# Kernel tuning notes

Measured on AMD Instinct MI355X. Metric: run time of the kernel, lower is better.

## Reference

```python
import jax, jax.numpy as jnp
import numpy as np
import math

D_MODEL = 1024
N_HEADS = 16
D_HEAD = D_MODEL // N_HEADS


def setup_inputs() -> dict:
    key = jax.random.key(0)
    ks = jax.random.split(key, 5)
    B, T, C = 4, 2048, D_MODEL
    s = 1.0 / math.sqrt(C)
    return {
        "x": jax.random.normal(ks[0], (B, T, C), dtype=jnp.float32),
        "qkv_w": jax.random.normal(ks[1], (3 * C, C), dtype=jnp.float32) * s,
        "qkv_b": jnp.zeros((3 * C,), dtype=jnp.float32),
        "out_w": jax.random.normal(ks[2], (C, C), dtype=jnp.float32) * s,
        "out_b": jnp.zeros((C,), dtype=jnp.float32),
    }


def reference(x, qkv_w, qkv_b, out_w, out_b):
    B, T, C = x.shape
    H, Dh = N_HEADS, D_HEAD
    qkv = x @ qkv_w.T + qkv_b              # [B,T,3C] (torch Linear: x W^T + b)
    q, k, v = jnp.split(qkv, 3, axis=-1)
    # [B,T,C] -> [B,H,T,Dh]
    q = q.reshape(B, T, H, Dh).transpose(0, 2, 1, 3)
    k = k.reshape(B, T, H, Dh).transpose(0, 2, 1, 3)
    v = v.reshape(B, T, H, Dh).transpose(0, 2, 1, 3)
    att = jnp.einsum("bhqd,bhkd->bhqk", q, k) / math.sqrt(Dh)
    causal = jnp.tril(jnp.ones((T, T), dtype=bool))  # True = keep
    att = jnp.where(causal, att, -jnp.inf)
    att = jax.nn.softmax(att, axis=-1)
    y = jnp.einsum("bhqk,bhkd->bhqd", att, v)
    y = y.transpose(0, 2, 1, 3).reshape(B, T, C)
    return y @ out_w.T + out_b
```

## Files before the change

### kernel.cpp

```cpp
#include <hip/hip_runtime.h>

typedef __attribute__((ext_vector_type(4))) float f32x4;
typedef __attribute__((ext_vector_type(16))) float f32x16;
typedef __attribute__((ext_vector_type(8))) __bf16 bf16x8;
typedef __attribute__((ext_vector_type(4))) __bf16 bf16x4;
typedef __attribute__((ext_vector_type(2))) unsigned u32x2;

#define MFMA_B16(a,b,c) __builtin_amdgcn_mfma_f32_16x16x32_bf16((a),(b),(c),0,0,0)
#define MFMA32(a,b,c)  __builtin_amdgcn_mfma_f32_32x32x16_bf16((a),(b),(c),0,0,0)

static constexpr int T_LEN  = 2048;
static constexpr int C_DIM  = 1024;
static constexpr int H_NUM  = 16;
static constexpr int D_HEADc = 64;
static constexpr float Q_PRESCALE = 0.125f * 1.4426950408889634f;

__device__ __forceinline__ void async16(const void* g, void* l) {
  __builtin_amdgcn_global_load_lds(
      (const __attribute__((address_space(1))) unsigned int*)g,
      (__attribute__((address_space(3))) unsigned int*)l, 16, 0, 0);
}

__device__ __forceinline__ unsigned cvtpk(float lo, float hi) {
  unsigned r;
  asm("v_cvt_pk_bf16_f32 %0, %1, %2" : "=v"(r) : "v"(lo), "v"(hi));
  return r;
}

__global__ __launch_bounds__(256) void cvt_kernel(const float* __restrict__ s,
                                                  __bf16* __restrict__ d, int n4) {
  int i = blockIdx.x * 256 + threadIdx.x;
  if (i >= n4) return;
  float4 f = reinterpret_cast<const float4*>(s)[i];
  bf16x4 o;
  o.x = (__bf16)f.x; o.y = (__bf16)f.y; o.z = (__bf16)f.z; o.w = (__bf16)f.w;
  reinterpret_cast<bf16x4*>(d)[i] = o;
}

__global__ __launch_bounds__(256) void gemm_qkv(const __bf16* __restrict__ A,
                                                const __bf16* __restrict__ W,
                                                const float* __restrict__ bias,
                                                __bf16* __restrict__ qb,
                                                __bf16* __restrict__ kb,
                                                __bf16* __restrict__ vb) {
  constexpr int K = 1024;
  __shared__ __bf16 As[128 * 64];
  __shared__ __bf16 Bs[128 * 64];
  const int tid = threadIdx.x;
  const int wid = tid >> 6, lane = tid & 63, l16 = lane & 15, lg = lane >> 4;
  const int r8 = lane >> 3, sl = lane & 7;
  const int r7 = l16 & 7;
  const int wm = wid >> 1, wn = wid & 1;
  const int m0 = blockIdx.x * 128, n0 = blockIdx.y * 128;

  f32x4 acc[4][4];
#pragma unroll
  for (int i = 0; i < 4; ++i)
#pragma unroll
    for (int j = 0; j < 4; ++j) acc[i][j] = f32x4{0.f, 0.f, 0.f, 0.f};

  for (int k0 = 0; k0 < K; k0 += 64) {
    __builtin_amdgcn_s_barrier();
#pragma unroll
    for (int it = 0; it < 4; ++it) {
      int chunk = it * 4 + wid;
      int row = chunk * 8 + r8;
      int scol = ((sl ^ (row & 7)) << 3);
      async16(A + (long)(m0 + row) * K + k0 + scol, &As[chunk * 512]);
      async16(W + (long)(n0 + row) * K + k0 + scol, &Bs[chunk * 512]);
    }
    asm volatile("s_waitcnt vmcnt(0)" ::: "memory");
    __builtin_amdgcn_s_barrier();
#pragma unroll
    for (int kt = 0; kt < 2; ++kt) {
      const int sw = ((((kt << 2) | lg) ^ r7) << 3);
      bf16x8 af[4], bfv[4];
#pragma unroll
      for (int mi = 0; mi < 4; ++mi)
        af[mi] = *reinterpret_cast<const bf16x8*>(&As[(wm * 64 + mi * 16 + l16) * 64 + sw]);
#pragma unroll
      for (int nt = 0; nt < 4; ++nt)
        bfv[nt] = *reinterpret_cast<const bf16x8*>(&Bs[(wn * 64 + nt * 16 + l16) * 64 + sw]);
#pragma unroll
      for (int mi = 0; mi < 4; ++mi)
#pragma unroll
        for (int nt = 0; nt < 4; ++nt)
          acc[mi][nt] = MFMA_B16(af[mi], bfv[nt], acc[mi][nt]);
    }
  }
#pragma unroll
  for (int mi = 0; mi < 4; ++mi)
#pragma unroll
    for (int nt = 0; nt < 4; ++nt)
#pragma unroll
      for (int r = 0; r < 4; ++r) {
        int m = m0 + wm * 64 + mi * 16 + lg * 4 + r;
        int n = n0 + wn * 64 + nt * 16 + l16;
        float val = acc[mi][nt][r] + bias[n];
        int which = n >> 10;
        int cc = n & 1023;
        int h = cc >> 6, d = cc & 63;
        long b = m >> 11;
        long t = m & 2047;
        if (which == 0) {
          qb[(((b * H_NUM + h) * T_LEN) + t) * D_HEADc + d] = (__bf16)(val * Q_PRESCALE);
        } else if (which == 1) {
          kb[(((b * H_NUM + h) * T_LEN) + t) * D_HEADc + d] = (__bf16)val;
        } else {
          vb[(((b * H_NUM + h) * D_HEADc) + d) * T_LEN + t] = (__bf16)val;
        }
      }
}

__global__ __launch_bounds__(256) void attn_kernel(const __bf16* __restrict__ q,
                                                   const __bf16* __restrict__ k,
                                                   const __bf16* __restrict__ vt,
                                                   __bf16* __restrict__ y) {
  __shared__ __bf16 Ks[2][64 * 64];
  __shared__ __bf16 Vs[2][64 * 64];
  const int tid = threadIdx.x;
  const int wid = tid >> 6, lane = tid & 63;
  const int l31 = lane & 31, hi = lane >> 5;
  const int r8 = lane >> 3, sl = lane & 7;
  const int r7 = l31 & 7;
  const int bid = blockIdx.x;
  const int qt = 15 - (bid >> 6);
  const int bh = bid & 63;
  const int q0 = qt * 128;
  const int qw = q0 + wid * 32;
  const int qglob = qw + l31;
  const __bf16* qg = q + (long)bh * T_LEN * D_HEADc;
  const __bf16* kg = k + (long)bh * T_LEN * D_HEADc;
  const __bf16* vg = vt + (long)bh * T_LEN * D_HEADc;

  bf16x8 qf[4];
#pragma unroll
  for (int dt = 0; dt < 4; ++dt)
    qf[dt] = *reinterpret_cast<const bf16x8*>(
        qg + (long)qglob * D_HEADc + dt * 16 + hi * 8);

  f32x16 o[2];
#pragma unroll
  for (int di = 0; di < 2; ++di)
#pragma unroll
    for (int r = 0; r < 16; ++r) o[di][r] = 0.f;
  float m = -3e38f, l = 0.f;

  auto stage = [&](int buf, int t) {
    const int k0s = t * 64;
#pragma unroll
    for (int it = 0; it < 2; ++it) {
      int chunk = it * 4 + wid;
      int row = chunk * 8 + r8;
      int scol = ((sl ^ (row & 7)) << 3);
      async16(kg + (long)(k0s + row) * D_HEADc + scol, &Ks[buf][chunk * 512]);
      async16(vg + (long)row * T_LEN + k0s + scol, &Vs[buf][chunk * 512]);
    }
  };

  const int ntiles = qt * 2 + 2;
  stage(0, 0);
  int cur = 0;
  for (int t = 0; t < ntiles; ++t) {
    if (t + 1 < ntiles) {
      stage(cur ^ 1, t + 1);
      asm volatile("s_waitcnt vmcnt(4)" ::: "memory");
    } else {
      asm volatile("s_waitcnt vmcnt(0)" ::: "memory");
    }
    __builtin_amdgcn_s_barrier();
    const int k0 = t * 64;
    if (k0 < qw + 32) {
      f32x16 s[2];
#pragma unroll
      for (int ki = 0; ki < 2; ++ki)
#pragma unroll
        for (int r = 0; r < 16; ++r) s[ki][r] = 0.f;
      __builtin_amdgcn_s_setprio(1);
#pragma unroll
      for (int dt = 0; dt < 4; ++dt) {
        const int swz = (((dt << 1) | hi) ^ r7) << 3;
        bf16x8 kf0 = *reinterpret_cast<const bf16x8*>(&Ks[cur][l31 * 64 + swz]);
        bf16x8 kf1 = *reinterpret_cast<const bf16x8*>(&Ks[cur][(32 + l31) * 64 + swz]);
        s[0] = MFMA32(kf0, qf[dt], s[0]);
        s[1] = MFMA32(kf1, qf[dt], s[1]);
      }
      __builtin_amdgcn_s_setprio(0);

      if (k0 + 63 > qw) {
#pragma unroll
        for (int r = 0; r < 16; ++r) {
          const int kb = (r & 3) + 8 * (r >> 2) + 4 * hi;
          if (k0 + kb > qglob) s[0][r] = -3e38f;
          if (k0 + 32 + kb > qglob) s[1][r] = -3e38f;
        }
      }
      float mx = -3e38f;
#pragma unroll
      for (int r = 0; r < 16; ++r) mx = fmaxf(mx, fmaxf(s[0][r], s[1][r]));
      mx = fmaxf(mx, __shfl_xor(mx, 32));
      if (!__all(mx <= m + 8.f)) {
        const float mn = fmaxf(m, mx);
        const float al = exp2f(m - mn);
        m = mn;
        l *= al;
#pragma unroll
        for (int di = 0; di < 2; ++di)
#pragma unroll
          for (int r = 0; r < 16; ++r) o[di][r] *= al;
      }
      float ls = 0.f;
      unsigned pb[4][4];
#pragma unroll
      for (int ki = 0; ki < 2; ++ki) {
#pragma unroll
        for (int r = 0; r < 16; ++r) {
          float e = exp2f(s[ki][r] - m);
          ls += e;
          s[ki][r] = e;
        }
        unsigned d0 = cvtpk(s[ki][0], s[ki][1]),   d1 = cvtpk(s[ki][2], s[ki][3]);
        unsigned d2 = cvtpk(s[ki][4], s[ki][5]),   d3 = cvtpk(s[ki][6], s[ki][7]);
        unsigned d4 = cvtpk(s[ki][8], s[ki][9]),   d5 = cvtpk(s[ki][10], s[ki][11]);
        unsigned d6 = cvtpk(s[ki][12], s[ki][13]), d7 = cvtpk(s[ki][14], s[ki][15]);
        u32x2 a = __builtin_amdgcn_permlane32_swap(d0, d2, false, false);
        u32x2 b = __builtin_amdgcn_permlane32_swap(d1, d3, false, false);
        pb[ki * 2][0] = a[0]; pb[ki * 2][1] = b[0];
        pb[ki * 2][2] = a[1]; pb[ki * 2][3] = b[1];
        u32x2 c = __builtin_amdgcn_permlane32_swap(d4, d6, false, false);
        u32x2 d = __builtin_amdgcn_permlane32_swap(d5, d7, false, false);
        pb[ki * 2 + 1][0] = c[0]; pb[ki * 2 + 1][1] = d[0];
        pb[ki * 2 + 1][2] = c[1]; pb[ki * 2 + 1][3] = d[1];
      }
      ls += __shfl_xor(ls, 32);
      l += ls;

      __builtin_amdgcn_s_setprio(1);
#pragma unroll
      for (int kt = 0; kt < 4; ++kt) {
        union { unsigned u[4]; bf16x8 v; } pu;
        pu.u[0] = pb[kt][0]; pu.u[1] = pb[kt][1];
        pu.u[2] = pb[kt][2]; pu.u[3] = pb[kt][3];
        const int swz = (((kt << 1) | hi) ^ r7) << 3;
        bf16x8 vf0 = *reinterpret_cast<const bf16x8*>(&Vs[cur][l31 * 64 + swz]);
        bf16x8 vf1 = *reinterpret_cast<const bf16x8*>(&Vs[cur][(32 + l31) * 64 + swz]);
        o[0] = MFMA32(vf0, pu.v, o[0]);
        o[1] = MFMA32(vf1, pu.v, o[1]);
      }
      __builtin_amdgcn_s_setprio(0);
    }
    __builtin_amdgcn_s_barrier();
    cur ^= 1;
  }

  const long bb = bh >> 4;
  const int h = bh & 15;
  const float inv = 1.f / l;
  const long row = bb * T_LEN + qglob;
#pragma unroll
  for (int di = 0; di < 2; ++di)
#pragma unroll
    for (int rr = 0; rr < 4; ++rr) {
      bf16x4 pk;
#pragma unroll
      for (int c = 0; c < 4; ++c) pk[c] = (__bf16)(o[di][rr * 4 + c] * inv);
      *reinterpret_cast<bf16x4*>(
          &y[row * C_DIM + h * D_HEADc + di * 32 + rr * 8 + hi * 4]) = pk;
    }
}

__global__ __launch_bounds__(256) void gemm_proj(const __bf16* __restrict__ A,
                                                 const __bf16* __restrict__ W,
                                                 const float* __restrict__ bias,
                                                 float* __restrict__ out) {
  constexpr int K = 1024;
  __shared__ __bf16 As[128 * 64];
  __shared__ __bf16 Bs[128 * 64];
  const int tid = threadIdx.x;
  const int wid = tid >> 6, lane = tid & 63, l16 = lane & 15, lg = lane >> 4;
  const int r8 = lane >> 3, sl = lane & 7;
  const int r7 = l16 & 7;
  const int wm = wid >> 1, wn = wid & 1;
  const int m0 = blockIdx.x * 128, n0 = blockIdx.y * 128;

  f32x4 acc[4][4];
#pragma unroll
  for (int i = 0; i < 4; ++i)
#pragma unroll
    for (int j = 0; j < 4; ++j) acc[i][j] = f32x4{0.f, 0.f, 0.f, 0.f};

  for (int k0 = 0; k0 < K; k0 += 64) {
    __builtin_amdgcn_s_barrier();
#pragma unroll
    for (int it = 0; it < 4; ++it) {
      int chunk = it * 4 + wid;
      int row = chunk * 8 + r8;
      int scol = ((sl ^ (row & 7)) << 3);
      async16(A + (long)(m0 + row) * K + k0 + scol, &As[chunk * 512]);
      async16(W + (long)(n0 + row) * K + k0 + scol, &Bs[chunk * 512]);
    }
    asm volatile("s_waitcnt vmcnt(0)" ::: "memory");
    __builtin_amdgcn_s_barrier();
#pragma unroll
    for (int kt = 0; kt < 2; ++kt) {
      const int sw = ((((kt << 2) | lg) ^ r7) << 3);
      bf16x8 af[4], bfv[4];
#pragma unroll
      for (int mi = 0; mi < 4; ++mi)
        af[mi] = *reinterpret_cast<const bf16x8*>(&As[(wm * 64 + mi * 16 + l16) * 64 + sw]);
#pragma unroll
      for (int nt = 0; nt < 4; ++nt)
        bfv[nt] = *reinterpret_cast<const bf16x8*>(&Bs[(wn * 64 + nt * 16 + l16) * 64 + sw]);
#pragma unroll
      for (int mi = 0; mi < 4; ++mi)
#pragma unroll
        for (int nt = 0; nt < 4; ++nt)
          acc[mi][nt] = MFMA_B16(af[mi], bfv[nt], acc[mi][nt]);
    }
  }
#pragma unroll
  for (int mi = 0; mi < 4; ++mi)
#pragma unroll
    for (int nt = 0; nt < 4; ++nt)
#pragma unroll
      for (int r = 0; r < 4; ++r) {
        long m = m0 + wm * 64 + mi * 16 + lg * 4 + r;
        int n = n0 + wn * 64 + nt * 16 + l16;
        out[m * C_DIM + n] = acc[mi][nt][r] + bias[n];
      }
}

extern "C" void kernel_launch(void* const* d_in, const int* in_sizes, int n_in,
                              void* d_out, int out_size, void* d_ws, size_t ws_size,
                              hipStream_t stream) {
  const float* x     = (const float*)d_in[0];
  const float* qkv_w = (const float*)d_in[1];
  const float* qkv_b = (const float*)d_in[2];
  const float* out_w = (const float*)d_in[3];
  const float* out_b = (const float*)d_in[4];
  float* out = (float*)d_out;

  const long NX  = 8192L * 1024;
  const long NWQ = 3072L * 1024;
  const long NWO = 1024L * 1024;
  const size_t need = (size_t)(5 * NX + NWQ + NWO) * 2;
  if (ws_size < need) return;

  __bf16* xb   = (__bf16*)d_ws;
  __bf16* wqkv = xb + NX;
  __bf16* wout = wqkv + NWQ;
  __bf16* qb   = wout + NWO;
  __bf16* kb   = qb + NX;
  __bf16* vb   = kb + NX;
  __bf16* yb   = vb + NX;

  cvt_kernel<<<(int)(NX / 4 / 256), 256, 0, stream>>>(x, xb, (int)(NX / 4));
  cvt_kernel<<<(int)(NWQ / 4 / 256), 256, 0, stream>>>(qkv_w, wqkv, (int)(NWQ / 4));
  cvt_kernel<<<(int)(NWO / 4 / 256), 256, 0, stream>>>(out_w, wout, (int)(NWO / 4));

  gemm_qkv<<<dim3(64, 24), 256, 0, stream>>>(xb, wqkv, qkv_b, qb, kb, vb);
  attn_kernel<<<dim3(1024), 256, 0, stream>>>(qb, kb, vb, yb);
  gemm_proj<<<dim3(64, 8), 256, 0, stream>>>(yb, wout, out_b, out);
}
```

Before: 196.4 us.

## Double attention query tile per block, fuse conversion kernels, tree-reduce softmax

Each attention warp now processes 64 query rows as two 32-row sub-blocks that share the K and V fragments loaded from LDS. The query tile per block grows to 256, which halves the grid and halves K/V staging traffic per query. The three fp32-to-bf16 conversion launches are merged into one kernel, and the softmax max and sum reductions become tree reductions. In exchange, register pressure roughly doubles, occupancy may fall, and the block count drops to 512, which may leave the causal workload less evenly balanced across CUs.

```diff
diff --git a/kernel.cpp b/kernel.cpp
--- a/kernel.cpp
+++ b/kernel.cpp
@@ -27,14 +27,21 @@
   return r;
 }
 
-__global__ __launch_bounds__(256) void cvt_kernel(const float* __restrict__ s,
-                                                  __bf16* __restrict__ d, int n4) {
+__global__ __launch_bounds__(256) void cvt3_kernel(const float* __restrict__ a, __bf16* __restrict__ da, int na,
+                                                   const float* __restrict__ b, __bf16* __restrict__ db, int nb,
+                                                   const float* __restrict__ c, __bf16* __restrict__ dc, int nc) {
   int i = blockIdx.x * 256 + threadIdx.x;
-  if (i >= n4) return;
-  float4 f = reinterpret_cast<const float4*>(s)[i];
+  const float* s;
+  __bf16* d;
+  long j;
+  if (i < na) { s = a; d = da; j = i; }
+  else if (i < na + nb) { s = b; d = db; j = i - na; }
+  else if (i < na + nb + nc) { s = c; d = dc; j = i - na - nb; }
+  else return;
+  float4 f = reinterpret_cast<const float4*>(s)[j];
   bf16x4 o;
   o.x = (__bf16)f.x; o.y = (__bf16)f.y; o.z = (__bf16)f.z; o.w = (__bf16)f.w;
-  reinterpret_cast<bf16x4*>(d)[i] = o;
+  reinterpret_cast<bf16x4*>(d)[j] = o;
 }
 
 __global__ __launch_bounds__(256) void gemm_qkv(const __bf16* __restrict__ A,
@@ -124,27 +131,29 @@
   const int r8 = lane >> 3, sl = lane & 7;
   const int r7 = l31 & 7;
   const int bid = blockIdx.x;
-  const int qt = 15 - (bid >> 6);
+  const int qt = 7 - (bid >> 6);
   const int bh = bid & 63;
-  const int q0 = qt * 128;
-  const int qw = q0 + wid * 32;
-  const int qglob = qw + l31;
+  const int q0 = qt * 256;
+  const int qw = q0 + wid * 64;
+  const int qgA = qw + l31;
+  const int qgB = qw + 32 + l31;
   const __bf16* qg = q + (long)bh * T_LEN * D_HEADc;
   const __bf16* kg = k + (long)bh * T_LEN * D_HEADc;
   const __bf16* vg = vt + (long)bh * T_LEN * D_HEADc;
 
-  bf16x8 qf[4];
-#pragma unroll
-  for (int dt = 0; dt < 4; ++dt)
-    qf[dt] = *reinterpret_cast<const bf16x8*>(
-        qg + (long)qglob * D_HEADc + dt * 16 + hi * 8);
-
-  f32x16 o[2];
+  bf16x8 qfA[4], qfB[4];
+#pragma unroll
+  for (int dt = 0; dt < 4; ++dt) {
+    qfA[dt] = *reinterpret_cast<const bf16x8*>(qg + (long)qgA * D_HEADc + dt * 16 + hi * 8);
+    qfB[dt] = *reinterpret_cast<const bf16x8*>(qg + (long)qgB * D_HEADc + dt * 16 + hi * 8);
+  }
+
+  f32x16 oA[2], oB[2];
 #pragma unroll
   for (int di = 0; di < 2; ++di)
 #pragma unroll
-    for (int r = 0; r < 16; ++r) o[di][r] = 0.f;
-  float m = -3e38f, l = 0.f;
+    for (int r = 0; r < 16; ++r) { oA[di][r] = 0.f; oB[di][r] = 0.f; }
+  float mA = -3e38f, lA = 0.f, mB = -3e38f, lB = 0.f;
 
   auto stage = [&](int buf, int t) {
     const int k0s = t * 64;
@@ -158,7 +167,66 @@
     }
   };
 
-  const int ntiles = qt * 2 + 2;
+  auto softmax_block = [&](f32x16* s, float& m, float& l, f32x16* o,
+                           unsigned (&pb)[4][4], int qgl, int qwl, int k0) {
+    if (k0 + 63 > qwl) {
+#pragma unroll
+      for (int r = 0; r < 16; ++r) {
+        const int kb = (r & 3) + 8 * (r >> 2) + 4 * hi;
+        if (k0 + kb > qgl) s[0][r] = -3e38f;
+        if (k0 + 32 + kb > qgl) s[1][r] = -3e38f;
+      }
+    }
+    float v8[8];
+#pragma unroll
+    for (int r = 0; r < 8; ++r)
+      v8[r] = fmaxf(fmaxf(s[0][r], s[0][r + 8]), fmaxf(s[1][r], s[1][r + 8]));
+#pragma unroll
+    for (int st = 4; st > 0; st >>= 1)
+#pragma unroll
+      for (int r = 0; r < st; ++r) v8[r] = fmaxf(v8[r], v8[r + st]);
+    float mx = fmaxf(v8[0], __shfl_xor(v8[0], 32));
+    if (!__all(mx <= m + 8.f)) {
+      const float mn = fmaxf(m, mx);
+      const float al = exp2f(m - mn);
+      m = mn;
+      l *= al;
+#pragma unroll
+      for (int di = 0; di < 2; ++di)
+#pragma unroll
+        for (int r = 0; r < 16; ++r) o[di][r] *= al;
+    }
+#pragma unroll
+    for (int ki = 0; ki < 2; ++ki)
+#pragma unroll
+      for (int r = 0; r < 16; ++r) s[ki][r] = exp2f(s[ki][r] - m);
+    float t8[8];
+#pragma unroll
+    for (int r = 0; r < 8; ++r)
+      t8[r] = (s[0][r] + s[0][r + 8]) + (s[1][r] + s[1][r + 8]);
+#pragma unroll
+    for (int st = 4; st > 0; st >>= 1)
+#pragma unroll
+      for (int r = 0; r < st; ++r) t8[r] += t8[r + st];
+    l += t8[0] + __shfl_xor(t8[0], 32);
+#pragma unroll
+    for (int ki = 0; ki < 2; ++ki) {
+      unsigned d0 = cvtpk(s[ki][0], s[ki][1]),   d1 = cvtpk(s[ki][2], s[ki][3]);
+      unsigned d2 = cvtpk(s[ki][4], s[ki][5]),   d3 = cvtpk(s[ki][6], s[ki][7]);
+      unsigned d4 = cvtpk(s[ki][8], s[ki][9]),   d5 = cvtpk(s[ki][10], s[ki][11]);
+      unsigned d6 = cvtpk(s[ki][12], s[ki][13]), d7 = cvtpk(s[ki][14], s[ki][15]);
+      u32x2 a2 = __builtin_amdgcn_permlane32_swap(d0, d2, false, false);
+      u32x2 b2 = __builtin_amdgcn_permlane32_swap(d1, d3, false, false);
+      pb[ki * 2][0] = a2[0]; pb[ki * 2][1] = b2[0];
+      pb[ki * 2][2] = a2[1]; pb[ki * 2][3] = b2[1];
+      u32x2 c2 = __builtin_amdgcn_permlane32_swap(d4, d6, false, false);
+      u32x2 e2 = __builtin_amdgcn_permlane32_swap(d5, d7, false, false);
+      pb[ki * 2 + 1][0] = c2[0]; pb[ki * 2 + 1][1] = e2[0];
+      pb[ki * 2 + 1][2] = c2[1]; pb[ki * 2 + 1][3] = e2[1];
+    }
+  };
+
+  const int ntiles = (qt + 1) * 4;
   stage(0, 0);
   int cur = 0;
   for (int t = 0; t < ntiles; ++t) {
@@ -170,82 +238,42 @@
     }
     __builtin_amdgcn_s_barrier();
     const int k0 = t * 64;
-    if (k0 < qw + 32) {
-      f32x16 s[2];
+    if (k0 < qw + 64) {
+      f32x16 sA[2], sB[2];
 #pragma unroll
       for (int ki = 0; ki < 2; ++ki)
 #pragma unroll
-        for (int r = 0; r < 16; ++r) s[ki][r] = 0.f;
+        for (int r = 0; r < 16; ++r) { sA[ki][r] = 0.f; sB[ki][r] = 0.f; }
       __builtin_amdgcn_s_setprio(1);
 #pragma unroll
       for (int dt = 0; dt < 4; ++dt) {
         const int swz = (((dt << 1) | hi) ^ r7) << 3;
         bf16x8 kf0 = *reinterpret_cast<const bf16x8*>(&Ks[cur][l31 * 64 + swz]);
         bf16x8 kf1 = *reinterpret_cast<const bf16x8*>(&Ks[cur][(32 + l31) * 64 + swz]);
-        s[0] = MFMA32(kf0, qf[dt], s[0]);
-        s[1] = MFMA32(kf1, qf[dt], s[1]);
+        sA[0] = MFMA32(kf0, qfA[dt], sA[0]);
+        sA[1] = MFMA32(kf1, qfA[dt], sA[1]);
+        sB[0] = MFMA32(kf0, qfB[dt], sB[0]);
+        sB[1] = MFMA32(kf1, qfB[dt], sB[1]);
       }
       __builtin_amdgcn_s_setprio(0);
 
-      if (k0 + 63 > qw) {
-#pragma unroll
-        for (int r = 0; r < 16; ++r) {
-          const int kb = (r & 3) + 8 * (r >> 2) + 4 * hi;
-          if (k0 + kb > qglob) s[0][r] = -3e38f;
-          if (k0 + 32 + kb > qglob) s[1][r] = -3e38f;
-        }
-      }
-      float mx = -3e38f;
-#pragma unroll
-      for (int r = 0; r < 16; ++r) mx = fmaxf(mx, fmaxf(s[0][r], s[1][r]));
-      mx = fmaxf(mx, __shfl_xor(mx, 32));
-      if (!__all(mx <= m + 8.f)) {
-        const float mn = fmaxf(m, mx);
-        const float al = exp2f(m - mn);
-        m = mn;
-        l *= al;
-#pragma unroll
-        for (int di = 0; di < 2; ++di)
-#pragma unroll
-          for (int r = 0; r < 16; ++r) o[di][r] *= al;
-      }
-      float ls = 0.f;
-      unsigned pb[4][4];
-#pragma unroll
-      for (int ki = 0; ki < 2; ++ki) {
-#pragma unroll
-        for (int r = 0; r < 16; ++r) {
-          float e = exp2f(s[ki][r] - m);
-          ls += e;
-          s[ki][r] = e;
-        }
-        unsigned d0 = cvtpk(s[ki][0], s[ki][1]),   d1 = cvtpk(s[ki][2], s[ki][3]);
-        unsigned d2 = cvtpk(s[ki][4], s[ki][5]),   d3 = cvtpk(s[ki][6], s[ki][7]);
-        unsigned d4 = cvtpk(s[ki][8], s[ki][9]),   d5 = cvtpk(s[ki][10], s[ki][11]);
-        unsigned d6 = cvtpk(s[ki][12], s[ki][13]), d7 = cvtpk(s[ki][14], s[ki][15]);
-        u32x2 a = __builtin_amdgcn_permlane32_swap(d0, d2, false, false);
-        u32x2 b = __builtin_amdgcn_permlane32_swap(d1, d3, false, false);
-        pb[ki * 2][0] = a[0]; pb[ki * 2][1] = b[0];
-        pb[ki * 2][2] = a[1]; pb[ki * 2][3] = b[1];
-        u32x2 c = __builtin_amdgcn_permlane32_swap(d4, d6, false, false);
-        u32x2 d = __builtin_amdgcn_permlane32_swap(d5, d7, false, false);
-        pb[ki * 2 + 1][0] = c[0]; pb[ki * 2 + 1][1] = d[0];
-        pb[ki * 2 + 1][2] = c[1]; pb[ki * 2 + 1][3] = d[1];
-      }
-      ls += __shfl_xor(ls, 32);
-      l += ls;
+      unsigned pbA[4][4], pbB[4][4];
+      softmax_block(sA, mA, lA, oA, pbA, qgA, qw, k0);
+      softmax_block(sB, mB, lB, oB, pbB, qgB, qw + 32, k0);
 
       __builtin_amdgcn_s_setprio(1);
 #pragma unroll
       for (int kt = 0; kt < 4; ++kt) {
-        union { unsigned u[4]; bf16x8 v; } pu;
-        pu.u[0] = pb[kt][0]; pu.u[1] = pb[kt][1];
-        pu.u[2] = pb[kt][2]; pu.u[3] = pb[kt][3];
+        union { unsigned u[4]; bf16x8 v; } puA, puB;
+#pragma unroll
+        for (int w = 0; w < 4; ++w) { puA.u[w] = pbA[kt][w]; puB.u[w] = pbB[kt][w]; }
         const int swz = (((kt << 1) | hi) ^ r7) << 3;
         bf16x8 vf0 = *reinterpret_cast<const bf16x8*>(&Vs[cur][l31 * 64 + swz]);
         bf16x8 vf1 = *reinterpret_cast<const bf16x8*>(&Vs[cur][(32 + l31) * 64 + swz]);
-        o[0] = MFMA32(vf0, pu.v, o[0]);
-        o[1] = MFMA32(vf1, pu.v, o[1]);
+        oA[0] = MFMA32(vf0, puA.v, oA[0]);
+        oA[1] = MFMA32(vf1, puA.v, oA[1]);
+        oB[0] = MFMA32(vf0, puB.v, oB[0]);
+        oB[1] = MFMA32(vf1, puB.v, oB[1]);
       }
       __builtin_amdgcn_s_setprio(0);
     }
@@ -255,17 +283,20 @@
 
   const long bb = bh >> 4;
   const int h = bh & 15;
-  const float inv = 1.f / l;
-  const long row = bb * T_LEN + qglob;
+  const float invA = 1.f / lA, invB = 1.f / lB;
+  const long rowA = bb * T_LEN + qgA, rowB = bb * T_LEN + qgB;
 #pragma unroll
   for (int di = 0; di < 2; ++di)
 #pragma unroll
     for (int rr = 0; rr < 4; ++rr) {
-      bf16x4 pk;
-#pragma unroll
-      for (int c = 0; c < 4; ++c) pk[c] = (__bf16)(o[di][rr * 4 + c] * inv);
-      *reinterpret_cast<bf16x4*>(
-          &y[row * C_DIM + h * D_HEADc + di * 32 + rr * 8 + hi * 4]) = pk;
+      bf16x4 pkA, pkB;
+#pragma unroll
+      for (int c = 0; c < 4; ++c) {
+        pkA[c] = (__bf16)(oA[di][rr * 4 + c] * invA);
+        pkB[c] = (__bf16)(oB[di][rr * 4 + c] * invB);
+      }
+      *reinterpret_cast<bf16x4*>(&y[rowA * C_DIM + h * D_HEADc + di * 32 + rr * 8 + hi * 4]) = pkA;
+      *reinterpret_cast<bf16x4*>(&y[rowB * C_DIM + h * D_HEADc + di * 32 + rr * 8 + hi * 4]) = pkB;
     }
 }
 
@@ -354,11 +385,10 @@
   __bf16* vb   = kb + NX;
   __bf16* yb   = vb + NX;
 
-  cvt_kernel<<<(int)(NX / 4 / 256), 256, 0, stream>>>(x, xb, (int)(NX / 4));
-  cvt_kernel<<<(int)(NWQ / 4 / 256), 256, 0, stream>>>(qkv_w, wqkv, (int)(NWQ / 4));
-  cvt_kernel<<<(int)(NWO / 4 / 256), 256, 0, stream>>>(out_w, wout, (int)(NWO / 4));
+  const int na = (int)(NX / 4), nb = (int)(NWQ / 4), nc = (int)(NWO / 4);
+  cvt3_kernel<<<(na + nb + nc + 255) / 256, 256, 0, stream>>>(x, xb, na, qkv_w, wqkv, nb, out_w, wout, nc);
 
   gemm_qkv<<<dim3(64, 24), 256, 0, stream>>>(xb, wqkv, qkv_b, qb, kb, vb);
-  attn_kernel<<<dim3(1024), 256, 0, stream>>>(qb, kb, vb, yb);
+  attn_kernel<<<dim3(512), 256, 0, stream>>>(qb, kb, vb, yb);
   gemm_proj<<<dim3(64, 8), 256, 0, stream>>>(yb, wout, out_b, out);
 }
```

Result: slower. 231.2 us (+17.7%).
